# Kernel optimization log

Measured on AMD Instinct MI355X. Metric: run time of the kernel, lower is better.

Reference implementation:

```python
import jax, jax.numpy as jnp
import numpy as np

N_RAYS, N_SAMPLES = 65536, 128


def setup_inputs() -> dict:
    key = jax.random.key(0)
    ks = jax.random.split(key, 6)
    sdf = jax.random.normal(ks[0], (N_RAYS, N_SAMPLES), dtype=jnp.float32)
    color = jax.random.uniform(ks[1], (N_RAYS, N_SAMPLES, 3), dtype=jnp.float32)
    # strictly increasing positive depths per ray
    dz = jax.random.uniform(ks[2], (N_RAYS, N_SAMPLES), dtype=jnp.float32) * 0.05 + 0.01
    z_vals = 0.1 + jnp.cumsum(dz, axis=-1)
    grad_theta = jax.random.normal(ks[3], (N_RAYS, N_SAMPLES, 3), dtype=jnp.float32)
    rd = jax.random.normal(ks[4], (N_RAYS, 3), dtype=jnp.float32)
    rays_d = rd / jnp.linalg.norm(rd, axis=-1, keepdims=True)
    s = jnp.array([64.0], dtype=jnp.float32)  # inv_s from SingleVarianceNetwork
    cos_anneal_ratio = jnp.float32(0.5)
    return {"sdf": sdf, "color": color, "z_vals": z_vals,
            "grad_theta": grad_theta, "rays_d": rays_d, "s": s,
            "cos_anneal_ratio": cos_anneal_ratio}


def reference(sdf, color, z_vals, grad_theta, rays_d, s, cos_anneal_ratio):
    # true cosine between ray dir and SDF gradient: [N, S]
    true_cos = jnp.sum(rays_d[:, None, :] * grad_theta, axis=-1)
    # annealed non-positive cosine (NeuS cos annealing)
    iter_cos = -(jax.nn.relu(-true_cos * 0.5 + 0.5) * (1.0 - cos_anneal_ratio)
                 + jax.nn.relu(-true_cos) * cos_anneal_ratio)
    dists = z_vals[:, 1:] - z_vals[:, :-1]                 # [N, S-1]
    est_next_sdf = sdf[..., :-1] + iter_cos[..., :-1] * dists * 0.5
    est_prev_sdf = sdf[..., :-1] - iter_cos[..., :-1] * dists * 0.5
    sv = s.reshape(())                                     # scalar inv_s
    prev_cdf = jax.nn.sigmoid(est_prev_sdf * sv)
    next_cdf = jax.nn.sigmoid(est_next_sdf * sv)
    alpha = jnp.clip((prev_cdf - next_cdf + 1e-5) / (prev_cdf + 1e-5), 0.0, 1.0)
    transmittance = jnp.cumprod(1.0 - alpha, axis=-1)      # [N, S-1]
    # faithful to source: a ZERO column is prepended to transmittance
    zcol = jnp.zeros((transmittance.shape[0], 1), transmittance.dtype)
    transmittance = jnp.concatenate([zcol, transmittance], axis=-1)  # [N, S]
    alpha = jnp.clip(jnp.concatenate([alpha, zcol], axis=-1), 0.0, 1.0)
    weight = transmittance * alpha                          # [N, S]
    pixel = jnp.sum(weight[..., None] * color, axis=-2)     # [N, 3]
    invdepth = jnp.sum(weight / z_vals, axis=-1)            # [N]
    return pixel, invdepth, weight
```

## Files before the change

kernel.cpp:

```cpp
#include <hip/hip_runtime.h>

#define N_RAYS 65536
#define N_SAMPLES 128

__device__ __forceinline__ float sigmoidf(float x) {
    return 1.0f / (1.0f + __expf(-x));
}

__global__ __launch_bounds__(256) void neus_kernel(
    const float* __restrict__ sdf,
    const float* __restrict__ color,
    const float* __restrict__ z_vals,
    const float* __restrict__ grad_theta,
    const float* __restrict__ rays_d,
    const float* __restrict__ s_ptr,
    const float* __restrict__ car_ptr,
    float* __restrict__ out_pixel,
    float* __restrict__ out_invdepth,
    float* __restrict__ out_weight)
{
    const int lane = threadIdx.x & 63;
    const int wave = threadIdx.x >> 6;
    const int ray  = blockIdx.x * 4 + wave;

    const float sv  = s_ptr[0];
    const float car = car_ptr[0];

    const float rdx = rays_d[ray * 3 + 0];
    const float rdy = rays_d[ray * 3 + 1];
    const float rdz = rays_d[ray * 3 + 2];

    const int s0   = 2 * lane;
    const int base = ray * N_SAMPLES;

    const float2 sd  = *(const float2*)(sdf    + base + s0);
    const float2 zz  = *(const float2*)(z_vals + base + s0);
    const float2 c01 = *(const float2*)(color      + (size_t)base * 3 + 6 * lane);
    const float2 c23 = *(const float2*)(color      + (size_t)base * 3 + 6 * lane + 2);
    const float2 c45 = *(const float2*)(color      + (size_t)base * 3 + 6 * lane + 4);
    const float2 g01 = *(const float2*)(grad_theta + (size_t)base * 3 + 6 * lane);
    const float2 g23 = *(const float2*)(grad_theta + (size_t)base * 3 + 6 * lane + 2);
    const float2 g45 = *(const float2*)(grad_theta + (size_t)base * 3 + 6 * lane + 4);

    const float z_next = __shfl_down(zz.x, 1, 64);

    const float tcA = rdx * g01.x + rdy * g01.y + rdz * g23.x;
    const float tcB = rdx * g23.y + rdy * g45.x + rdz * g45.y;

    const float one_m_car = 1.0f - car;
    auto iter_cos = [&](float tc) -> float {
        float a = fmaxf(-tc * 0.5f + 0.5f, 0.0f);
        float b = fmaxf(-tc, 0.0f);
        return -(a * one_m_car + b * car);
    };
    const float icA = iter_cos(tcA);
    const float icB = iter_cos(tcB);

    const float dA = zz.y - zz.x;
    const float dB = z_next - zz.y;

    auto alpha_f = [&](float sdv, float ic, float d) -> float {
        float h  = ic * d * 0.5f;
        float pc = sigmoidf((sdv - h) * sv);
        float nc = sigmoidf((sdv + h) * sv);
        float a  = (pc - nc + 1e-5f) / (pc + 1e-5f);
        return fminf(fmaxf(a, 0.0f), 1.0f);
    };

    const float alphaA = alpha_f(sd.x, icA, dA);
    const float alphaB = (lane == 63) ? 0.0f : alpha_f(sd.y, icB, dB);

    const float omA = 1.0f - alphaA;
    const float omB = 1.0f - alphaB;

    float scan = omA * omB;
    #pragma unroll
    for (int off = 1; off < 64; off <<= 1) {
        float v = __shfl_up(scan, off, 64);
        if (lane >= off) scan *= v;
    }
    float excl = __shfl_up(scan, 1, 64);
    if (lane == 0) excl = 1.0f;

    const float TA = excl;
    const float TB = excl * omA;

    const float wA = (lane == 0) ? 0.0f : TA * alphaA;
    const float wB = TB * alphaB;

    float pr  = wA * c01.x + wB * c23.y;
    float pg  = wA * c01.y + wB * c45.x;
    float pb  = wA * c23.x + wB * c45.y;
    float inv = wA / zz.x + wB / zz.y;

    #pragma unroll
    for (int off = 32; off > 0; off >>= 1) {
        pr  += __shfl_xor(pr,  off, 64);
        pg  += __shfl_xor(pg,  off, 64);
        pb  += __shfl_xor(pb,  off, 64);
        inv += __shfl_xor(inv, off, 64);
    }

    *(float2*)(out_weight + base + s0) = make_float2(wA, wB);

    if (lane == 0) {
        out_pixel[ray * 3 + 0] = pr;
        out_pixel[ray * 3 + 1] = pg;
        out_pixel[ray * 3 + 2] = pb;
        out_invdepth[ray]      = inv;
    }
}

extern "C" void kernel_launch(void* const* d_in, const int* in_sizes, int n_in,
                              void* d_out, int out_size, void* d_ws, size_t ws_size,
                              hipStream_t stream) {
    const float* sdf        = (const float*)d_in[0];
    const float* color      = (const float*)d_in[1];
    const float* z_vals     = (const float*)d_in[2];
    const float* grad_theta = (const float*)d_in[3];
    const float* rays_d     = (const float*)d_in[4];
    const float* s_ptr      = (const float*)d_in[5];
    const float* car_ptr    = (const float*)d_in[6];

    float* out          = (float*)d_out;
    float* out_pixel    = out;
    float* out_invdepth = out + (size_t)N_RAYS * 3;
    float* out_weight   = out + (size_t)N_RAYS * 4;

    dim3 block(256);
    dim3 grid(N_RAYS / 4);

    neus_kernel<<<grid, block, 0, stream>>>(
        sdf, color, z_vals, grad_theta, rays_d, s_ptr, car_ptr,
        out_pixel, out_invdepth, out_weight);
}
```

Before: 267.1 us.

## Stage grad and color through LDS via global_load_lds, 32 lanes per ray

Each 32-lane half-wave now handles one ray with four samples per lane, and a block covers eight rays. The interleaved 3-channel grad_theta and color arrays are staged into LDS with 16-byte direct global-to-LDS loads, replacing strided float2 global loads. The color load is issued after grad is consumed so it overlaps the alpha and scan math. The scan and reduction shrink to width 32, and the divides become fast-math __fdividef calls. The cost is manual waitcnt handling, a shared LDS buffer reused for both tensors without a barrier, and slightly less precise division.

New measurement: 273.8 us. 2.5% more time.

```diff
diff --git a/kernel.cpp b/kernel.cpp
--- a/kernel.cpp
+++ b/kernel.cpp
@@ -2,12 +2,20 @@
 
 #define N_RAYS 65536
 #define N_SAMPLES 128
+#define RPB 8
+
+__device__ __forceinline__ void gll16(const float* g, float* l) {
+    __builtin_amdgcn_global_load_lds(
+        (const __attribute__((address_space(1))) void*)g,
+        (__attribute__((address_space(3))) void*)l,
+        16, 0, 0);
+}
 
 __device__ __forceinline__ float sigmoidf(float x) {
-    return 1.0f / (1.0f + __expf(-x));
+    return __fdividef(1.0f, 1.0f + __expf(-x));
 }
 
-__global__ __launch_bounds__(256) void neus_kernel(
+__global__ __launch_bounds__(256, 8) void neus_kernel(
     const float* __restrict__ sdf,
     const float* __restrict__ color,
     const float* __restrict__ z_vals,
@@ -19,91 +27,131 @@
     float* __restrict__ out_invdepth,
     float* __restrict__ out_weight)
 {
-    const int lane = threadIdx.x & 63;
-    const int wave = threadIdx.x >> 6;
-    const int ray  = blockIdx.x * 4 + wave;
+    __shared__ __align__(16) float lds[RPB * N_SAMPLES * 3];
 
-    const float sv  = s_ptr[0];
-    const float car = car_ptr[0];
+    const int tid = threadIdx.x;
+    const int l   = tid & 31;
+    const int r   = tid >> 5;
+    const int wv  = tid >> 6;
+    const int l64 = tid & 63;
+    const int ray = blockIdx.x * RPB + r;
 
+    const size_t base  = (size_t)ray * N_SAMPLES;
+    const size_t base3 = (size_t)blockIdx.x * (RPB * N_SAMPLES * 3);
+
+    {
+        const float* g = grad_theta + base3;
+        #pragma unroll
+        for (int k = 0; k < 3; ++k) {
+            const int q = wv * 3 + k;
+            gll16(g + q * 256 + l64 * 4, &lds[q * 256]);
+        }
+    }
+
+    const float4 sd = *(const float4*)(sdf    + base + 4 * l);
+    const float4 zz = *(const float4*)(z_vals + base + 4 * l);
     const float rdx = rays_d[ray * 3 + 0];
     const float rdy = rays_d[ray * 3 + 1];
     const float rdz = rays_d[ray * 3 + 2];
+    const float sv  = s_ptr[0];
+    const float car = car_ptr[0];
+    const float omc = 1.0f - car;
 
-    const int s0   = 2 * lane;
-    const int base = ray * N_SAMPLES;
+    asm volatile("s_waitcnt vmcnt(0)" ::: "memory");
 
-    const float2 sd  = *(const float2*)(sdf    + base + s0);
-    const float2 zz  = *(const float2*)(z_vals + base + s0);
-    const float2 c01 = *(const float2*)(color      + (size_t)base * 3 + 6 * lane);
-    const float2 c23 = *(const float2*)(color      + (size_t)base * 3 + 6 * lane + 2);
-    const float2 c45 = *(const float2*)(color      + (size_t)base * 3 + 6 * lane + 4);
-    const float2 g01 = *(const float2*)(grad_theta + (size_t)base * 3 + 6 * lane);
-    const float2 g23 = *(const float2*)(grad_theta + (size_t)base * 3 + 6 * lane + 2);
-    const float2 g45 = *(const float2*)(grad_theta + (size_t)base * 3 + 6 * lane + 4);
+    const int fo = r * 384 + 12 * l;
+    const float4 gA = *(const float4*)&lds[fo + 0];
+    const float4 gB = *(const float4*)&lds[fo + 4];
+    const float4 gC = *(const float4*)&lds[fo + 8];
 
-    const float z_next = __shfl_down(zz.x, 1, 64);
+    asm volatile("s_waitcnt lgkmcnt(0)" ::: "memory");
 
-    const float tcA = rdx * g01.x + rdy * g01.y + rdz * g23.x;
-    const float tcB = rdx * g23.y + rdy * g45.x + rdz * g45.y;
+    {
+        const float* c = color + base3;
+        #pragma unroll
+        for (int k = 0; k < 3; ++k) {
+            const int q = wv * 3 + k;
+            gll16(c + q * 256 + l64 * 4, &lds[q * 256]);
+        }
+    }
 
-    const float one_m_car = 1.0f - car;
+    const float tc0 = rdx * gA.x + rdy * gA.y + rdz * gA.z;
+    const float tc1 = rdx * gA.w + rdy * gB.x + rdz * gB.y;
+    const float tc2 = rdx * gB.z + rdy * gB.w + rdz * gC.x;
+    const float tc3 = rdx * gC.y + rdy * gC.z + rdz * gC.w;
+
     auto iter_cos = [&](float tc) -> float {
-        float a = fmaxf(-tc * 0.5f + 0.5f, 0.0f);
+        float a = fmaxf(fmaf(tc, -0.5f, 0.5f), 0.0f);
         float b = fmaxf(-tc, 0.0f);
-        return -(a * one_m_car + b * car);
+        return -(a * omc + b * car);
     };
-    const float icA = iter_cos(tcA);
-    const float icB = iter_cos(tcB);
+    const float ic0 = iter_cos(tc0);
+    const float ic1 = iter_cos(tc1);
+    const float ic2 = iter_cos(tc2);
+    const float ic3 = iter_cos(tc3);
 
-    const float dA = zz.y - zz.x;
-    const float dB = z_next - zz.y;
+    const float zn = __shfl_down(zz.x, 1, 32);
+    const float d0 = zz.y - zz.x;
+    const float d1 = zz.z - zz.y;
+    const float d2 = zz.w - zz.z;
+    const float d3 = zn   - zz.w;
 
     auto alpha_f = [&](float sdv, float ic, float d) -> float {
         float h  = ic * d * 0.5f;
         float pc = sigmoidf((sdv - h) * sv);
         float nc = sigmoidf((sdv + h) * sv);
-        float a  = (pc - nc + 1e-5f) / (pc + 1e-5f);
+        float a  = __fdividef(pc - nc + 1e-5f, pc + 1e-5f);
         return fminf(fmaxf(a, 0.0f), 1.0f);
     };
+    const float a0 = alpha_f(sd.x, ic0, d0);
+    const float a1 = alpha_f(sd.y, ic1, d1);
+    const float a2 = alpha_f(sd.z, ic2, d2);
+    const float a3 = (l == 31) ? 0.0f : alpha_f(sd.w, ic3, d3);
 
-    const float alphaA = alpha_f(sd.x, icA, dA);
-    const float alphaB = (lane == 63) ? 0.0f : alpha_f(sd.y, icB, dB);
+    const float om0 = 1.0f - a0;
+    const float om1 = 1.0f - a1;
+    const float om2 = 1.0f - a2;
+    const float om3 = 1.0f - a3;
 
-    const float omA = 1.0f - alphaA;
-    const float omB = 1.0f - alphaB;
+    float scan = om0 * om1 * om2 * om3;
+    #pragma unroll
+    for (int off = 1; off < 32; off <<= 1) {
+        float v = __shfl_up(scan, off, 32);
+        if (l >= off) scan *= v;
+    }
+    float excl = __shfl_up(scan, 1, 32);
+    if (l == 0) excl = 1.0f;
 
-    float scan = omA * omB;
-    #pragma unroll
-    for (int off = 1; off < 64; off <<= 1) {
-        float v = __shfl_up(scan, off, 64);
-        if (lane >= off) scan *= v;
-    }
-    float excl = __shfl_up(scan, 1, 64);
-    if (lane == 0) excl = 1.0f;
+    float t  = excl;
+    const float w0 = (l == 0) ? 0.0f : t * a0;
+    t *= om0; const float w1 = t * a1;
+    t *= om1; const float w2 = t * a2;
+    t *= om2; const float w3 = t * a3;
 
-    const float TA = excl;
-    const float TB = excl * omA;
+    float inv = w0 * __fdividef(1.0f, zz.x) + w1 * __fdividef(1.0f, zz.y)
+              + w2 * __fdividef(1.0f, zz.z) + w3 * __fdividef(1.0f, zz.w);
 
-    const float wA = (lane == 0) ? 0.0f : TA * alphaA;
-    const float wB = TB * alphaB;
+    asm volatile("s_waitcnt vmcnt(0)" ::: "memory");
 
-    float pr  = wA * c01.x + wB * c23.y;
-    float pg  = wA * c01.y + wB * c45.x;
-    float pb  = wA * c23.x + wB * c45.y;
-    float inv = wA / zz.x + wB / zz.y;
+    const float4 cA = *(const float4*)&lds[fo + 0];
+    const float4 cB = *(const float4*)&lds[fo + 4];
+    const float4 cC = *(const float4*)&lds[fo + 8];
+
+    *(float4*)(out_weight + base + 4 * l) = make_float4(w0, w1, w2, w3);
+
+    float pr = w0 * cA.x + w1 * cA.w + w2 * cB.z + w3 * cC.y;
+    float pg = w0 * cA.y + w1 * cB.x + w2 * cB.w + w3 * cC.z;
+    float pb = w0 * cA.z + w1 * cB.y + w2 * cC.x + w3 * cC.w;
 
     #pragma unroll
-    for (int off = 32; off > 0; off >>= 1) {
-        pr  += __shfl_xor(pr,  off, 64);
-        pg  += __shfl_xor(pg,  off, 64);
-        pb  += __shfl_xor(pb,  off, 64);
-        inv += __shfl_xor(inv, off, 64);
+    for (int off = 16; off > 0; off >>= 1) {
+        pr  += __shfl_xor(pr,  off, 32);
+        pg  += __shfl_xor(pg,  off, 32);
+        pb  += __shfl_xor(pb,  off, 32);
+        inv += __shfl_xor(inv, off, 32);
     }
 
-    *(float2*)(out_weight + base + s0) = make_float2(wA, wB);
-
-    if (lane == 0) {
+    if (l == 0) {
         out_pixel[ray * 3 + 0] = pr;
         out_pixel[ray * 3 + 1] = pg;
         out_pixel[ray * 3 + 2] = pb;
@@ -128,7 +176,7 @@
     float* out_weight   = out + (size_t)N_RAYS * 4;
 
     dim3 block(256);
-    dim3 grid(N_RAYS / 4);
+    dim3 grid(N_RAYS / RPB);
 
     neus_kernel<<<grid, block, 0, stream>>>(
         sdf, color, z_vals, grad_theta, rays_d, s_ptr, car_ptr,
```
